# Kernel optimization log

Measured on AMD Instinct MI355X. Metric: run time of the kernel, lower is better.

Reference implementation:

```python
import jax, jax.numpy as jnp
import numpy as np

B, C, S, K, HEADS, P = 2, 64, 112, 7, 4, 3
DH = C // HEADS

def _na_idx(L, k):
    # NATTEN-style clamped windows: each query attends to k in-bounds neighbors
    i = np.arange(L)
    s = np.clip(i - k // 2, 0, L - k)
    nbr = s[:, None] + np.arange(k)[None, :]      # (L,k) absolute neighbor index
    rel = nbr - i[:, None] + (k - 1)              # (L,k) rel-pos-bias index in [0,2k-2]
    return jnp.asarray(nbr), jnp.asarray(rel)

def _ln(x, g, b, eps=1e-5):
    m = jnp.mean(x, -1, keepdims=True)
    v = jnp.mean(jnp.square(x - m), -1, keepdims=True)
    return (x - m) * jax.lax.rsqrt(v + eps) * g + b

def _conv(x, w, b):
    y = jax.lax.conv_general_dilated(x, w, (1, 1), [(P // 2, P // 2)] * 2,
                                     dimension_numbers=('NCHW', 'OIHW', 'NCHW'))
    return jnp.transpose(y + b[None, :, None, None], (0, 2, 3, 1))  # NHWC

def setup_inputs():
    key = jax.random.key(0)
    ks = jax.random.split(key, 24)
    r = lambda i, shape, s=0.02: jax.random.normal(ks[i], shape, jnp.float32) * s
    return {
        'xq': jax.random.normal(ks[0], (B, C, S, S), jnp.float32),
        'xkv': jax.random.normal(ks[1], (B, C, S, S), jnp.float32),
        'conv_w_s': r(2, (C, C, P, P)), 'conv_b_s': r(3, (C,), 0.01),
        'conv_w_l': r(4, (C, C, P, P)), 'conv_b_l': r(5, (C,), 0.01),
        'g_s': jnp.ones((C,), jnp.float32), 'b_s': jnp.zeros((C,), jnp.float32),
        'g_l': jnp.ones((C,), jnp.float32), 'b_l': jnp.zeros((C,), jnp.float32),
        'Wq': r(6, (C, C)), 'bq': r(7, (C,), 0.01),
        'Wk': r(8, (C, C)), 'bk': r(9, (C,), 0.01),
        'Wv': r(10, (C, C)), 'bv': r(11, (C,), 0.01),
        'Wo': r(12, (C, C)), 'bo': r(13, (C,), 0.01),
        'rpb': r(14, (HEADS, 2 * K - 1, 2 * K - 1)),
        'g_n': jnp.ones((C,), jnp.float32), 'b_n': jnp.zeros((C,), jnp.float32),
        'W1': r(15, (C, 2 * C)), 'b1': r(16, (2 * C,), 0.01),
        'W2': r(17, (2 * C, C)), 'b2': r(18, (C,), 0.01),
    }

def reference(xq, xkv, conv_w_s, conv_b_s, conv_w_l, conv_b_l, g_s, b_s, g_l, b_l,
              Wq, bq, Wk, bk, Wv, bv, Wo, bo, rpb, g_n, b_n, W1, b1, W2, b2):
    emb_q = _conv(xq, conv_w_s, conv_b_s)     # (B,H,W,C) overlap patch embed (q branch)
    emb_kv = _conv(xkv, conv_w_l, conv_b_l)   # (B,H,W,C)
    Hh, Ww = emb_q.shape[1], emb_q.shape[2]
    qn = _ln(emb_q, g_s, b_s)
    kvn = _ln(emb_kv, g_l, b_l)
    q = (qn @ Wq + bq).reshape(B, Hh, Ww, HEADS, DH)
    k = (kvn @ Wk + bk).reshape(B, Hh, Ww, HEADS, DH)
    v = (kvn @ Wv + bv).reshape(B, Hh, Ww, HEADS, DH)
    ni, ri = _na_idx(Hh, K)
    nj, rj = _na_idx(Ww, K)

    def gather(t):  # (B,H,W,h,d) -> (B,H,W,K*K,h,d) neighborhood windows
        t = t[:, ni]                                 # (B,H,K,W,h,d)
        t = t[:, :, :, nj]                           # (B,H,K,W,K,h,d)
        t = jnp.transpose(t, (0, 1, 3, 2, 4, 5, 6))  # (B,H,W,K,K,h,d)
        return t.reshape(B, Hh, Ww, K * K, HEADS, DH)

    kg, vg = gather(k), gather(v)
    logits = jnp.einsum('bijhd,bijnhd->bhijn', q, kg) * (DH ** -0.5)
    bias = rpb[:, ri]                                # (h,H,K,2K-1)
    bias = bias[:, :, :, rj]                         # (h,H,K,W,K)
    bias = jnp.transpose(bias, (0, 1, 3, 2, 4)).reshape(HEADS, Hh, Ww, K * K)
    attn = jax.nn.softmax(logits + bias[None], axis=-1)
    out = jnp.einsum('bhijn,bijnhd->bijhd', attn, vg).reshape(B, Hh, Ww, C)
    att = out @ Wo + bo + emb_kv                     # residual with kv embedding
    x = _ln(att, g_n, b_n)
    x = jax.nn.gelu(x @ W1 + b1, approximate=False) @ W2 + b2 + att
    return jnp.transpose(x, (0, 3, 1, 2))            # (B,C,H,W)
```

## Files before the change

### kernel.cpp

```cpp
#include <hip/hip_runtime.h>
#include <math.h>

#define SS 112
#define HW (SS*SS)
#define NPIX (2*HW)

typedef __bf16 v8bf __attribute__((ext_vector_type(8)));
typedef short  v8s  __attribute__((ext_vector_type(8)));
typedef float  v4f  __attribute__((ext_vector_type(4)));

__device__ __forceinline__ unsigned short f2bf(float f){
  unsigned u = __builtin_bit_cast(unsigned, f);
  u = (u + 0x7fffu + ((u >> 16) & 1u)) >> 16;
  return (unsigned short)u;
}
__device__ __forceinline__ unsigned cvt_pk_bf16(float lo, float hi){
  unsigned r;
  asm("v_cvt_pk_bf16_f32 %0, %1, %2" : "=v"(r) : "v"(lo), "v"(hi));
  return r;
}
__device__ __forceinline__ v8bf zero8(){
  v8s z = {0,0,0,0,0,0,0,0};
  return __builtin_bit_cast(v8bf, z);
}
__device__ __forceinline__ float gelu_fast(float x){
  float u = fmaf(0.044715f*x, x, 1.0f);
  float z = fminf(2.3021178f * x * u, 80.0f);
  float s = exp2f(z);
  return x * s * __builtin_amdgcn_rcpf(s + 1.0f);
}

__device__ __forceinline__ void pack_wconv(const float* __restrict__ w,
                                           unsigned short* __restrict__ WB, int idx){
  int lane = idx & 63, tslot = (idx >> 6) & 3, kk = idx >> 8;
  int tap = kk >> 1;
  int ic0 = ((kk & 1) << 5) + ((lane >> 4) << 3);
  int oc  = tslot*16 + (lane & 15);
  union { unsigned short u[8]; uint4 q; } pk;
  #pragma unroll
  for (int i = 0; i < 8; ++i) pk.u[i] = f2bf(w[(oc*64 + ic0 + i)*9 + tap]);
  ((uint4*)WB)[idx] = pk.q;
}
__device__ __forceinline__ void pack_wlin(const float* __restrict__ W,
                                          unsigned short* __restrict__ WB,
                                          int N, int idx){
  int lane = idx & 63;
  int tmp = idx >> 6;
  int tiles = N >> 4;
  int tslot = tmp % tiles;
  int kk = tmp / tiles;
  int k0 = kk*32 + ((lane >> 4) << 3);
  int oc = tslot*16 + (lane & 15);
  union { unsigned short u[8]; uint4 q; } pk;
  #pragma unroll
  for (int i = 0; i < 8; ++i) pk.u[i] = f2bf(W[(size_t)(k0 + i)*N + oc]);
  ((uint4*)WB)[idx] = pk.q;
}

__global__ __launch_bounds__(256) void k_prep(
    const float* __restrict__ xq, const float* __restrict__ xkv,
    const float* __restrict__ cws, const float* __restrict__ cwl,
    const float* __restrict__ Wq, const float* __restrict__ Wk,
    const float* __restrict__ Wv, const float* __restrict__ Wo,
    const float* __restrict__ W1, const float* __restrict__ W2,
    const float* __restrict__ rpb,
    unsigned short* __restrict__ WBs, unsigned short* __restrict__ WBl,
    unsigned short* __restrict__ WBq, unsigned short* __restrict__ WBk,
    unsigned short* __restrict__ WBv, unsigned short* __restrict__ WBo,
    unsigned short* __restrict__ WB1, unsigned short* __restrict__ WB2,
    float* __restrict__ rpb2g,
    unsigned short* __restrict__ xTq, unsigned short* __restrict__ xTkv)
{
  __shared__ float tile[64][68];
  const int blk = blockIdx.x, t = threadIdx.x;
  if (blk < 55){
    if      (blk < 18) pack_wconv(cws, WBs, blk*256 + t);
    else if (blk < 36) pack_wconv(cwl, WBl, (blk-18)*256 + t);
    else if (blk < 38) pack_wlin(Wq, WBq, 64,  (blk-36)*256 + t);
    else if (blk < 40) pack_wlin(Wk, WBk, 64,  (blk-38)*256 + t);
    else if (blk < 42) pack_wlin(Wv, WBv, 64,  (blk-40)*256 + t);
    else if (blk < 44) pack_wlin(Wo, WBo, 64,  (blk-42)*256 + t);
    else if (blk < 48) pack_wlin(W1, WB1, 128, (blk-44)*256 + t);
    else if (blk < 52) pack_wlin(W2, WB2, 64,  (blk-48)*256 + t);
    else {
      int idx = (blk-52)*256 + t;
      if (idx < 4*169) rpb2g[idx] = rpb[idx] * 1.4426950408889634f;
    }
    return;
  }
  const int blk2 = blk - 55;
  const int inst = blk2 >= (NPIX/64) ? 1 : 0;
  const float* x = inst ? xkv : xq;
  unsigned short* xT = inst ? xTkv : xTq;
  const int base = (blk2 - inst*(NPIX/64)) * 64;
  const int b = base / HW;
  const int r0 = base - b*HW;
  {
    const int c = t >> 2, xo = (t & 3) << 4;
    const float* src = x + ((size_t)(b*64 + c))*HW + r0 + xo;
    float4 v0 = ((const float4*)src)[0];
    float4 v1 = ((const float4*)src)[1];
    float4 v2 = ((const float4*)src)[2];
    float4 v3 = ((const float4*)src)[3];
    float* dst = &tile[c][xo];
    ((float4*)dst)[0] = v0; ((float4*)dst)[1] = v1;
    ((float4*)dst)[2] = v2; ((float4*)dst)[3] = v3;
  }
  __syncthreads();
  {
    const int px = t >> 2, co = (t & 3) << 4;
    union { unsigned short u[16]; uint4 q[2]; } pk;
    #pragma unroll
    for (int i = 0; i < 16; ++i) pk.u[i] = f2bf(tile[co + i][px]);
    uint4* dst = (uint4*)(xT + ((size_t)(base + px))*64 + co);
    dst[0] = pk.q[0]; dst[1] = pk.q[1];
  }
}

__global__ __launch_bounds__(256) void k_conv_all(
    const unsigned short* __restrict__ xTq, const unsigned short* __restrict__ xTkv,
    const unsigned short* __restrict__ WBs, const unsigned short* __restrict__ WBl,
    const float* __restrict__ cbs, const float* __restrict__ g_s, const float* __restrict__ b_s,
    const float* __restrict__ cbl, const float* __restrict__ g_l, const float* __restrict__ b_l,
    const unsigned short* __restrict__ WBq, const float* __restrict__ bq_,
    const unsigned short* __restrict__ WBk, const float* __restrict__ bk_,
    const unsigned short* __restrict__ WBv, const float* __restrict__ bv_,
    unsigned short* __restrict__ qb, unsigned short* __restrict__ kb,
    unsigned short* __restrict__ vT, float* __restrict__ emb)
{
  __shared__ unsigned short nlds[4][16*64];
  const int tid = threadIdx.x;
  const int wid = tid >> 6, l = tid & 63;
  const int g = l >> 4, c = l & 15;
  const int HALF = NPIX/64;
  const int inst = blockIdx.x >= HALF ? 1 : 0;
  const int P0 = ((blockIdx.x - inst*HALF)*4 + wid) * 16;

  const unsigned short* xT  = inst ? xTkv : xTq;
  const unsigned short* WBc = inst ? WBl : WBs;
  const float* cb    = inst ? cbl : cbs;
  const float* gamma = inst ? g_l : g_s;
  const float* beta  = inst ? b_l : b_s;

  const int p = P0 + c;
  const int b = p / HW, r = p - b*HW;
  const int py = r / SS, pxx = r - py*SS;
  const int pb64 = b*HW;

  float cbv[4], gv[4], bev[4];
  #pragma unroll
  for (int t = 0; t < 4; ++t){
    cbv[t] = cb[c + 16*t]; gv[t] = gamma[c + 16*t]; bev[t] = beta[c + 16*t];
  }

  v4f acc[4];
  #pragma unroll
  for (int t = 0; t < 4; ++t) acc[t] = (v4f){cbv[t], cbv[t], cbv[t], cbv[t]};

  const int icg = g << 3;
  #pragma unroll
  for (int kk = 0; kk < 18; ++kk){
    const int tap = kk >> 1;
    const int dy = tap/3 - 1, dx = tap - (tap/3)*3 - 1;
    const int icof = ((kk & 1) << 5) + icg;
    int yy = py + dy, xx = pxx + dx;
    bool ok = ((unsigned)yy < SS) && ((unsigned)xx < SS);
    v8bf a = zero8();
    if (ok) a = *(const v8bf*)(xT + ((size_t)(pb64 + yy*SS + xx))*64 + icof);
    #pragma unroll
    for (int t = 0; t < 4; ++t){
      v8bf bfr = *(const v8bf*)(WBc + ((size_t)((kk*4 + t)*64 + l))*8);
      acc[t] = __builtin_amdgcn_mfma_f32_16x16x32_bf16(a, bfr, acc[t], 0, 0, 0);
    }
  }

  if (inst){
    #pragma unroll
    for (int t = 0; t < 4; ++t)
      #pragma unroll
      for (int r2 = 0; r2 < 4; ++r2)
        emb[((size_t)(P0 + 4*g + r2))*64 + c + 16*t] = acc[t][r2];
  }

  {
    float mean[4], inv[4];
    #pragma unroll
    for (int r2 = 0; r2 < 4; ++r2){
      float s = acc[0][r2] + acc[1][r2] + acc[2][r2] + acc[3][r2];
      s += __shfl_xor(s, 1, 64); s += __shfl_xor(s, 2, 64);
      s += __shfl_xor(s, 4, 64); s += __shfl_xor(s, 8, 64);
      mean[r2] = s * (1.f/64.f);
      float d0 = acc[0][r2] - mean[r2], d1 = acc[1][r2] - mean[r2];
      float d2 = acc[2][r2] - mean[r2], d3 = acc[3][r2] - mean[r2];
      float vs = d0*d0 + d1*d1 + d2*d2 + d3*d3;
      vs += __shfl_xor(vs, 1, 64); vs += __shfl_xor(vs, 2, 64);
      vs += __shfl_xor(vs, 4, 64); vs += __shfl_xor(vs, 8, 64);
      inv[r2] = rsqrtf(vs * (1.f/64.f) + 1e-5f);
    }
    #pragma unroll
    for (int t = 0; t < 4; ++t){
      int c16 = 2*t + (c >> 3);
      #pragma unroll
      for (int r2 = 0; r2 < 4; r2 += 2){
        int row0 = 4*g + r2, row1 = row0 + 1;
        float n0 = (acc[t][r2]   - mean[r2])   * inv[r2]   * gv[t] + bev[t];
        float n1 = (acc[t][r2+1] - mean[r2+1]) * inv[r2+1] * gv[t] + bev[t];
        unsigned w = cvt_pk_bf16(n0, n1);
        nlds[wid][row0*64 + (((c16 ^ (row0 & 7)) << 3) | (c & 7))] = (unsigned short)(w & 0xffffu);
        nlds[wid][row1*64 + (((c16 ^ (row1 & 7)) << 3) | (c & 7))] = (unsigned short)(w >> 16);
      }
    }
  }

  #pragma unroll
  for (int which = 0; which < 2; ++which){
    if (which == 1 && !inst) break;
    const unsigned short* WB = which ? WBv : (inst ? WBk : WBq);
    const float* bias        = which ? bv_ : (inst ? bk_ : bq_);

    float pb[4];
    #pragma unroll
    for (int t = 0; t < 4; ++t) pb[t] = bias[c + 16*t];
    v4f pa[4];
    #pragma unroll
    for (int t = 0; t < 4; ++t) pa[t] = (v4f){pb[t], pb[t], pb[t], pb[t]};

    #pragma unroll
    for (int kk = 0; kk < 2; ++kk){
      v8bf av = *(const v8bf*)(nlds[wid] + c*64 + (((kk*4 + g) ^ (c & 7)) << 3));
      #pragma unroll
      for (int t = 0; t < 4; ++t){
        v8bf bfr = *(const v8bf*)(WB + ((size_t)((kk*4 + t)*64 + l))*8);
        pa[t] = __builtin_amdgcn_mfma_f32_16x16x32_bf16(av, bfr, pa[t], 0, 0, 0);
      }
    }
    if (which == 0){
      unsigned short* outp = inst ? kb : qb;
      #pragma unroll
      for (int t = 0; t < 4; ++t)
        #pragma unroll
        for (int r2 = 0; r2 < 4; r2 += 2){
          unsigned w = cvt_pk_bf16(pa[t][r2], pa[t][r2+1]);
          outp[((size_t)(P0 + 4*g + r2))*64 + c + 16*t]     = (unsigned short)(w & 0xffffu);
          outp[((size_t)(P0 + 4*g + r2+1))*64 + c + 16*t]   = (unsigned short)(w >> 16);
        }
    } else {
      #pragma unroll
      for (int t = 0; t < 4; ++t){
        uint2 w2;
        w2.x = cvt_pk_bf16(pa[t][0], pa[t][1]);
        w2.y = cvt_pk_bf16(pa[t][2], pa[t][3]);
        *(uint2*)(vT + (size_t)(c + 16*t)*NPIX + (P0 + 4*g)) = w2;
      }
    }
  }
}

__global__ __launch_bounds__(256) void k_natten_mfma(
    const unsigned short* __restrict__ q, const unsigned short* __restrict__ k,
    const unsigned short* __restrict__ vT, const float* __restrict__ rpb2g,
    unsigned short* __restrict__ out)
{
  const int l = threadIdx.x & 63;
  const int h = threadIdx.x >> 6;
  const int p0 = blockIdx.x * 16;
  const int b = p0 / HW, r0 = p0 - b*HW;
  const int i = r0 / SS, j0 = r0 - i*SS;
  const int c = l & 15, g = l >> 4;

  const int si = min(max(i - 3, 0), SS - 7);
  const int aj = (min(max(j0 - 3, 0), SS - 22)) & ~7;
  const int oi = si - i + 6;
  const int pbase = b*HW;

  const int j   = j0 + c;
  const int sjp = min(max(j - 3, 0), SS - 7);
  const int adj = 8*g + (aj - sjp);
  const float* bp = rpb2g + h*169 + oi*13 + (8*g + aj - j + 6);

  v8bf bq = zero8();
  if (g < 2) bq = *(const v8bf*)(q + (size_t)(p0 + c)*64 + h*16 + 8*g);

  float lt[14][4];
  const int arow = 8*(c >> 2) + (c & 3);
  #pragma unroll
  for (int tau = 0; tau < 14; ++tau){
    const int t = tau >> 1;
    int kpix = pbase + (si + t)*SS + aj + arow + 4*(tau & 1);
    kpix = min(kpix, NPIX - 1);
    v8bf ak = zero8();
    if (g < 2) ak = *(const v8bf*)(k + (size_t)kpix*64 + h*16 + 8*g);
    v4f a0 = {0.f,0.f,0.f,0.f};
    a0 = __builtin_amdgcn_mfma_f32_16x16x32_bf16(ak, bq, a0, 0, 0, 0);
    lt[tau][0]=a0[0]; lt[tau][1]=a0[1]; lt[tau][2]=a0[2]; lt[tau][3]=a0[3];
  }

  const float SC = 0.3606737602222409f;
  float mx4[4] = {-3e38f,-3e38f,-3e38f,-3e38f};
  #pragma unroll
  for (int tau = 0; tau < 14; ++tau){
    const int t = tau >> 1;
    #pragma unroll
    for (int r = 0; r < 4; ++r){
      const int cc = 4*(tau & 1) + r;
      float bias = bp[t*13 + cc];
      float lg = fmaf(lt[tau][r], SC, bias);
      lt[tau][r] = ((unsigned)(adj + cc) <= 6u) ? lg : -1e30f;
      mx4[r] = fmaxf(mx4[r], lt[tau][r]);
    }
  }
  float mx = fmaxf(fmaxf(mx4[0], mx4[1]), fmaxf(mx4[2], mx4[3]));
  mx = fmaxf(mx, __shfl_xor(mx, 16, 64));
  mx = fmaxf(mx, __shfl_xor(mx, 32, 64));
  float es4[4] = {0.f,0.f,0.f,0.f};
  #pragma unroll
  for (int tau = 0; tau < 14; ++tau)
    #pragma unroll
    for (int r = 0; r < 4; ++r){
      float p = exp2f(lt[tau][r] - mx);
      lt[tau][r] = p;
      es4[r] += p;
    }
  float es = (es4[0] + es4[1]) + (es4[2] + es4[3]);
  es += __shfl_xor(es, 16, 64);
  es += __shfl_xor(es, 32, 64);
  const float inv = 1.0f / es;

  const unsigned short* vrow = vT + (size_t)(h*16 + c)*NPIX;
  v4f oacc = {0.f,0.f,0.f,0.f};
  #pragma unroll
  for (int t = 0; t < 7; ++t){
    union { unsigned w[4]; v8bf bf; } pa;
    pa.w[0] = cvt_pk_bf16(lt[2*t][0]*inv,   lt[2*t][1]*inv);
    pa.w[1] = cvt_pk_bf16(lt[2*t][2]*inv,   lt[2*t][3]*inv);
    pa.w[2] = cvt_pk_bf16(lt[2*t+1][0]*inv, lt[2*t+1][1]*inv);
    pa.w[3] = cvt_pk_bf16(lt[2*t+1][2]*inv, lt[2*t+1][3]*inv);
    int vpixb = pbase + (si + t)*SS + aj + 8*g;
    vpixb = min(vpixb, NPIX - 8);
    v8bf bv = *(const v8bf*)(vrow + vpixb);
    oacc = __builtin_amdgcn_mfma_f32_16x16x32_bf16(pa.bf, bv, oacc, 0, 0, 0);
  }

  #pragma unroll
  for (int r = 0; r < 4; r += 2){
    unsigned w = cvt_pk_bf16(oacc[r], oacc[r+1]);
    out[(size_t)(p0 + 4*g + r)*64 + h*16 + c]     = (unsigned short)(w & 0xffffu);
    out[(size_t)(p0 + 4*g + r+1)*64 + h*16 + c]   = (unsigned short)(w >> 16);
  }
}

__global__ __launch_bounds__(256) void k_out_mfma(
    const unsigned short* __restrict__ ao, const float* __restrict__ emb,
    const unsigned short* __restrict__ WBo, const float* __restrict__ bo,
    const float* __restrict__ gn, const float* __restrict__ bn,
    const unsigned short* __restrict__ WB1, const float* __restrict__ b1,
    const unsigned short* __restrict__ WB2, const float* __restrict__ b2,
    float* __restrict__ outp)
{
  __shared__ unsigned short ylds[4][16*64];
  __shared__ unsigned short hlds[4][16*128];
  const int tid = threadIdx.x;
  const int wid = tid >> 6, l = tid & 63;
  const int g = l >> 4, c = l & 15;
  const int P0 = (blockIdx.x*4 + wid) * 16;
  const int b = P0 / HW;
  const int ijb = P0 - b*HW;

  v4f att[4];
  #pragma unroll
  for (int t = 0; t < 4; ++t){
    float bb = bo[c + 16*t];
    #pragma unroll
    for (int r = 0; r < 4; ++r)
      att[t][r] = bb + emb[((size_t)(P0 + 4*g + r))*64 + c + 16*t];
  }
  #pragma unroll
  for (int kk = 0; kk < 2; ++kk){
    v8bf a = *(const v8bf*)(ao + (size_t)(P0 + c)*64 + kk*32 + 8*g);
    #pragma unroll
    for (int t = 0; t < 4; ++t){
      v8bf bfr = *(const v8bf*)(WBo + ((size_t)((kk*4 + t)*64 + l))*8);
      att[t] = __builtin_amdgcn_mfma_f32_16x16x32_bf16(a, bfr, att[t], 0, 0, 0);
    }
  }

  {
    float gv[4], bev[4];
    #pragma unroll
    for (int t = 0; t < 4; ++t){ gv[t] = gn[c + 16*t]; bev[t] = bn[c + 16*t]; }
    float mean[4], inv[4];
    #pragma unroll
    for (int r = 0; r < 4; ++r){
      float s = att[0][r] + att[1][r] + att[2][r] + att[3][r];
      s += __shfl_xor(s, 1, 64); s += __shfl_xor(s, 2, 64);
      s += __shfl_xor(s, 4, 64); s += __shfl_xor(s, 8, 64);
      mean[r] = s * (1.f/64.f);
      float d0 = att[0][r] - mean[r], d1 = att[1][r] - mean[r];
      float d2 = att[2][r] - mean[r], d3 = att[3][r] - mean[r];
      float vs = d0*d0 + d1*d1 + d2*d2 + d3*d3;
      vs += __shfl_xor(vs, 1, 64); vs += __shfl_xor(vs, 2, 64);
      vs += __shfl_xor(vs, 4, 64); vs += __shfl_xor(vs, 8, 64);
      inv[r] = rsqrtf(vs * (1.f/64.f) + 1e-5f);
    }
    #pragma unroll
    for (int t = 0; t < 4; ++t){
      int c16 = 2*t + (c >> 3);
      #pragma unroll
      for (int r = 0; r < 4; r += 2){
        int row0 = 4*g + r, row1 = row0 + 1;
        float n0 = (att[t][r]   - mean[r])   * inv[r]   * gv[t] + bev[t];
        float n1 = (att[t][r+1] - mean[r+1]) * inv[r+1] * gv[t] + bev[t];
        unsigned w = cvt_pk_bf16(n0, n1);
        ylds[wid][row0*64 + (((c16 ^ (row0 & 7)) << 3) | (c & 7))] = (unsigned short)(w & 0xffffu);
        ylds[wid][row1*64 + (((c16 ^ (row1 & 7)) << 3) | (c & 7))] = (unsigned short)(w >> 16);
      }
    }
  }

  v4f hc[8];
  #pragma unroll
  for (int tt = 0; tt < 8; ++tt){
    float bb = b1[c + 16*tt];
    hc[tt] = (v4f){bb,bb,bb,bb};
  }
  #pragma unroll
  for (int kk = 0; kk < 2; ++kk){
    v8bf a = *(const v8bf*)(ylds[wid] + c*64 + (((kk*4 + g) ^ (c & 7)) << 3));
    #pragma unroll
    for (int tt = 0; tt < 8; ++tt){
      v8bf bfr = *(const v8bf*)(WB1 + ((size_t)((kk*8 + tt)*64 + l))*8);
      hc[tt] = __builtin_amdgcn_mfma_f32_16x16x32_bf16(a, bfr, hc[tt], 0, 0, 0);
    }
  }
  #pragma unroll
  for (int tt = 0; tt < 8; ++tt){
    int chunk = 2*tt + (c >> 3);
    #pragma unroll
    for (int r = 0; r < 4; r += 2){
      int row0 = 4*g + r, row1 = row0 + 1;
      int swz0 = (chunk & 8) | ((chunk & 7) ^ (row0 & 7));
      int swz1 = (chunk & 8) | ((chunk & 7) ^ (row1 & 7));
      unsigned w = cvt_pk_bf16(gelu_fast(hc[tt][r]), gelu_fast(hc[tt][r+1]));
      hlds[wid][row0*128 + swz0*8 + (c & 7)] = (unsigned short)(w & 0xffffu);
      hlds[wid][row1*128 + swz1*8 + (c & 7)] = (unsigned short)(w >> 16);
    }
  }

  v4f xc[4];
  #pragma unroll
  for (int t = 0; t < 4; ++t){
    float bb = b2[c + 16*t];
    #pragma unroll
    for (int r = 0; r < 4; ++r)
      xc[t][r] = bb + att[t][r];
  }
  #pragma unroll
  for (int kk = 0; kk < 4; ++kk){
    int chunk = 4*kk + g;
    int swz = (chunk & 8) | ((chunk & 7) ^ (c & 7));
    v8bf a = *(const v8bf*)(hlds[wid] + c*128 + swz*8);
    #pragma unroll
    for (int t = 0; t < 4; ++t){
      v8bf bfr = *(const v8bf*)(WB2 + ((size_t)((kk*4 + t)*64 + l))*8);
      xc[t] = __builtin_amdgcn_mfma_f32_16x16x32_bf16(a, bfr, xc[t], 0, 0, 0);
    }
  }
  #pragma unroll
  for (int t = 0; t < 4; ++t)
    #pragma unroll
    for (int r = 0; r < 4; ++r)
      outp[((size_t)(b*64 + c + 16*t))*HW + ijb + 4*g + r] = xc[t][r];
}

extern "C" void kernel_launch(void* const* d_in, const int* in_sizes, int n_in,
                              void* d_out, int out_size, void* d_ws, size_t ws_size,
                              hipStream_t stream) {
  const float* xq  = (const float*)d_in[0];
  const float* xkv = (const float*)d_in[1];
  const float* cws = (const float*)d_in[2];
  const float* cbs = (const float*)d_in[3];
  const float* cwl = (const float*)d_in[4];
  const float* cbl = (const float*)d_in[5];
  const float* g_s = (const float*)d_in[6];
  const float* b_s = (const float*)d_in[7];
  const float* g_l = (const float*)d_in[8];
  const float* b_l = (const float*)d_in[9];
  const float* Wq  = (const float*)d_in[10];
  const float* bq  = (const float*)d_in[11];
  const float* Wk  = (const float*)d_in[12];
  const float* bk  = (const float*)d_in[13];
  const float* Wv  = (const float*)d_in[14];
  const float* bv  = (const float*)d_in[15];
  const float* Wo  = (const float*)d_in[16];
  const float* bo  = (const float*)d_in[17];
  const float* rpb = (const float*)d_in[18];
  const float* g_n = (const float*)d_in[19];
  const float* b_n = (const float*)d_in[20];
  const float* W1  = (const float*)d_in[21];
  const float* b1  = (const float*)d_in[22];
  const float* W2  = (const float*)d_in[23];
  const float* b2  = (const float*)d_in[24];

  unsigned short* xTq  = (unsigned short*)d_ws;
  unsigned short* xTkv = xTq  + (size_t)NPIX*64;
  unsigned short* WBs  = xTkv + (size_t)NPIX*64;
  unsigned short* WBl  = WBs  + 36864;
  unsigned short* WBq  = WBl  + 36864;
  unsigned short* WBk  = WBq  + 4096;
  unsigned short* WBv  = WBk  + 4096;
  unsigned short* WBo  = WBv  + 4096;
  unsigned short* WB1  = WBo  + 4096;
  unsigned short* WB2  = WB1  + 8192;
  unsigned short* qb   = WB2  + 8192;
  unsigned short* kb   = qb   + (size_t)NPIX*64;
  unsigned short* vT   = kb   + (size_t)NPIX*64;
  unsigned short* aob  = vT   + (size_t)NPIX*64;
  float* emb   = (float*)(aob + (size_t)NPIX*64);
  float* rpb2a = emb + (size_t)NPIX*64;
  float* rpb2g = rpb2a + 64;

  hipLaunchKernelGGL(k_prep, dim3(55 + NPIX/32), dim3(256), 0, stream,
      xq, xkv, cws, cwl, Wq, Wk, Wv, Wo, W1, W2, rpb,
      WBs, WBl, WBq, WBk, WBv, WBo, WB1, WB2, rpb2g, xTq, xTkv);

  hipLaunchKernelGGL(k_conv_all, dim3(NPIX/32), dim3(256), 0, stream,
      xTq, xTkv, WBs, WBl,
      cbs, g_s, b_s, cbl, g_l, b_l,
      WBq, bq, WBk, bk, WBv, bv,
      qb, kb, vT, emb);

  hipLaunchKernelGGL(k_natten_mfma, dim3(NPIX/16), dim3(256), 0, stream,
      qb, kb, vT, rpb2g, aob);

  hipLaunchKernelGGL(k_out_mfma, dim3(NPIX/64), dim3(256), 0, stream,
      aob, emb, WBo, bo, g_n, b_n, WB1, b1, WB2, b2, (float*)d_out);
}
```

Measured before the change: 75.01 us.

## Fuse neighborhood attention with output projection and MLP into one kernel

```diff
diff --git a/kernel.cpp b/kernel.cpp
--- a/kernel.cpp
+++ b/kernel.cpp
@@ -29,6 +29,16 @@
   float s = exp2f(z);
   return x * s * __builtin_amdgcn_rcpf(s + 1.0f);
 }
+
+struct Params {
+  const float *xq, *xkv, *cws, *cwl, *Wq, *Wk, *Wv, *Wo, *W1, *W2, *rpb;
+  const float *cbs, *g_s, *b_s, *cbl, *g_l, *b_l;
+  const float *bq, *bk, *bv, *bo, *gn, *bn, *b1, *b2;
+  unsigned short *WBs, *WBl, *WBq, *WBk, *WBv, *WBo, *WB1, *WB2;
+  float *rpb2g;
+  unsigned short *xTq, *xTkv, *qb, *kb, *vT;
+  float *emb, *outp;
+};
 
 __device__ __forceinline__ void pack_wconv(const float* __restrict__ w,
                                            unsigned short* __restrict__ WB, int idx){
@@ -57,90 +67,70 @@
   ((uint4*)WB)[idx] = pk.q;
 }
 
-__global__ __launch_bounds__(256) void k_prep(
-    const float* __restrict__ xq, const float* __restrict__ xkv,
-    const float* __restrict__ cws, const float* __restrict__ cwl,
-    const float* __restrict__ Wq, const float* __restrict__ Wk,
-    const float* __restrict__ Wv, const float* __restrict__ Wo,
-    const float* __restrict__ W1, const float* __restrict__ W2,
-    const float* __restrict__ rpb,
-    unsigned short* __restrict__ WBs, unsigned short* __restrict__ WBl,
-    unsigned short* __restrict__ WBq, unsigned short* __restrict__ WBk,
-    unsigned short* __restrict__ WBv, unsigned short* __restrict__ WBo,
-    unsigned short* __restrict__ WB1, unsigned short* __restrict__ WB2,
-    float* __restrict__ rpb2g,
-    unsigned short* __restrict__ xTq, unsigned short* __restrict__ xTkv)
+__global__ __launch_bounds__(256) void k_prep_s(Params P)
 {
   __shared__ float tile[64][68];
-  const int blk = blockIdx.x, t = threadIdx.x;
-  if (blk < 55){
-    if      (blk < 18) pack_wconv(cws, WBs, blk*256 + t);
-    else if (blk < 36) pack_wconv(cwl, WBl, (blk-18)*256 + t);
-    else if (blk < 38) pack_wlin(Wq, WBq, 64,  (blk-36)*256 + t);
-    else if (blk < 40) pack_wlin(Wk, WBk, 64,  (blk-38)*256 + t);
-    else if (blk < 42) pack_wlin(Wv, WBv, 64,  (blk-40)*256 + t);
-    else if (blk < 44) pack_wlin(Wo, WBo, 64,  (blk-42)*256 + t);
-    else if (blk < 48) pack_wlin(W1, WB1, 128, (blk-44)*256 + t);
-    else if (blk < 52) pack_wlin(W2, WB2, 64,  (blk-48)*256 + t);
+  const int u = blockIdx.x, tid = threadIdx.x;
+  if (u >= 784){
+    const int pu = u - 784;
+    if      (pu < 18) pack_wconv(P.cws, P.WBs, pu*256 + tid);
+    else if (pu < 36) pack_wconv(P.cwl, P.WBl, (pu-18)*256 + tid);
+    else if (pu < 38) pack_wlin(P.Wq, P.WBq, 64,  (pu-36)*256 + tid);
+    else if (pu < 40) pack_wlin(P.Wk, P.WBk, 64,  (pu-38)*256 + tid);
+    else if (pu < 42) pack_wlin(P.Wv, P.WBv, 64,  (pu-40)*256 + tid);
+    else if (pu < 44) pack_wlin(P.Wo, P.WBo, 64,  (pu-42)*256 + tid);
+    else if (pu < 48) pack_wlin(P.W1, P.WB1, 128, (pu-44)*256 + tid);
+    else if (pu < 52) pack_wlin(P.W2, P.WB2, 64,  (pu-48)*256 + tid);
     else {
-      int idx = (blk-52)*256 + t;
-      if (idx < 4*169) rpb2g[idx] = rpb[idx] * 1.4426950408889634f;
+      int idx = (pu-52)*256 + tid;
+      if (idx < 4*169) P.rpb2g[idx] = P.rpb[idx] * 1.4426950408889634f;
     }
     return;
   }
-  const int blk2 = blk - 55;
-  const int inst = blk2 >= (NPIX/64) ? 1 : 0;
-  const float* x = inst ? xkv : xq;
-  unsigned short* xT = inst ? xTkv : xTq;
-  const int base = (blk2 - inst*(NPIX/64)) * 64;
+  const int inst = u >= 392 ? 1 : 0;
+  const float* x = inst ? P.xkv : P.xq;
+  unsigned short* xT = inst ? P.xTkv : P.xTq;
+  const int base = (u - inst*392) * 64;
   const int b = base / HW;
   const int r0 = base - b*HW;
   {
-    const int c = t >> 2, xo = (t & 3) << 4;
-    const float* src = x + ((size_t)(b*64 + c))*HW + r0 + xo;
+    const int cc = tid >> 2, xo = (tid & 3) << 4;
+    const float* src = x + ((size_t)(b*64 + cc))*HW + r0 + xo;
     float4 v0 = ((const float4*)src)[0];
     float4 v1 = ((const float4*)src)[1];
     float4 v2 = ((const float4*)src)[2];
     float4 v3 = ((const float4*)src)[3];
-    float* dst = &tile[c][xo];
+    float* dst = &tile[cc][xo];
     ((float4*)dst)[0] = v0; ((float4*)dst)[1] = v1;
     ((float4*)dst)[2] = v2; ((float4*)dst)[3] = v3;
   }
   __syncthreads();
   {
-    const int px = t >> 2, co = (t & 3) << 4;
-    union { unsigned short u[16]; uint4 q[2]; } pk;
-    #pragma unroll
-    for (int i = 0; i < 16; ++i) pk.u[i] = f2bf(tile[co + i][px]);
+    const int px = tid >> 2, co = (tid & 3) << 4;
+    union { unsigned short uu[16]; uint4 q[2]; } pk;
+    #pragma unroll
+    for (int i = 0; i < 16; ++i) pk.uu[i] = f2bf(tile[co + i][px]);
     uint4* dst = (uint4*)(xT + ((size_t)(base + px))*64 + co);
     dst[0] = pk.q[0]; dst[1] = pk.q[1];
   }
 }
 
-__global__ __launch_bounds__(256) void k_conv_all(
-    const unsigned short* __restrict__ xTq, const unsigned short* __restrict__ xTkv,
-    const unsigned short* __restrict__ WBs, const unsigned short* __restrict__ WBl,
-    const float* __restrict__ cbs, const float* __restrict__ g_s, const float* __restrict__ b_s,
-    const float* __restrict__ cbl, const float* __restrict__ g_l, const float* __restrict__ b_l,
-    const unsigned short* __restrict__ WBq, const float* __restrict__ bq_,
-    const unsigned short* __restrict__ WBk, const float* __restrict__ bk_,
-    const unsigned short* __restrict__ WBv, const float* __restrict__ bv_,
-    unsigned short* __restrict__ qb, unsigned short* __restrict__ kb,
-    unsigned short* __restrict__ vT, float* __restrict__ emb)
+__global__ __launch_bounds__(256) void k_conv_s(Params P)
 {
-  __shared__ unsigned short nlds[4][16*64];
+  __shared__ unsigned short nlds4[4][1024];
   const int tid = threadIdx.x;
   const int wid = tid >> 6, l = tid & 63;
   const int g = l >> 4, c = l & 15;
-  const int HALF = NPIX/64;
-  const int inst = blockIdx.x >= HALF ? 1 : 0;
-  const int P0 = ((blockIdx.x - inst*HALF)*4 + wid) * 16;
-
-  const unsigned short* xT  = inst ? xTkv : xTq;
-  const unsigned short* WBc = inst ? WBl : WBs;
-  const float* cb    = inst ? cbl : cbs;
-  const float* gamma = inst ? g_l : g_s;
-  const float* beta  = inst ? b_l : b_s;
+  unsigned short* nlds = nlds4[wid];
+  const int u = blockIdx.x;
+  const int inst = u >= 392 ? 1 : 0;
+  const int P0 = ((u - inst*392)*4 + wid) * 16;
+
+  const unsigned short* xT  = inst ? P.xTkv : P.xTq;
+  const unsigned short* WBc = inst ? P.WBl : P.WBs;
+  const float* cb    = inst ? P.cbl : P.cbs;
+  const float* gamma = inst ? P.g_l : P.g_s;
+  const float* beta  = inst ? P.b_l : P.b_s;
 
   const int p = P0 + c;
   const int b = p / HW, r = p - b*HW;
@@ -179,7 +169,7 @@
     for (int t = 0; t < 4; ++t)
       #pragma unroll
       for (int r2 = 0; r2 < 4; ++r2)
-        emb[((size_t)(P0 + 4*g + r2))*64 + c + 16*t] = acc[t][r2];
+        P.emb[((size_t)(P0 + 4*g + r2))*64 + c + 16*t] = acc[t][r2];
   }
 
   {
@@ -206,8 +196,8 @@
         float n0 = (acc[t][r2]   - mean[r2])   * inv[r2]   * gv[t] + bev[t];
         float n1 = (acc[t][r2+1] - mean[r2+1]) * inv[r2+1] * gv[t] + bev[t];
         unsigned w = cvt_pk_bf16(n0, n1);
-        nlds[wid][row0*64 + (((c16 ^ (row0 & 7)) << 3) | (c & 7))] = (unsigned short)(w & 0xffffu);
-        nlds[wid][row1*64 + (((c16 ^ (row1 & 7)) << 3) | (c & 7))] = (unsigned short)(w >> 16);
+        nlds[row0*64 + (((c16 ^ (row0 & 7)) << 3) | (c & 7))] = (unsigned short)(w & 0xffffu);
+        nlds[row1*64 + (((c16 ^ (row1 & 7)) << 3) | (c & 7))] = (unsigned short)(w >> 16);
       }
     }
   }
@@ -215,8 +205,8 @@
   #pragma unroll
   for (int which = 0; which < 2; ++which){
     if (which == 1 && !inst) break;
-    const unsigned short* WB = which ? WBv : (inst ? WBk : WBq);
-    const float* bias        = which ? bv_ : (inst ? bk_ : bq_);
+    const unsigned short* WB = which ? P.WBv : (inst ? P.WBk : P.WBq);
+    const float* bias        = which ? P.bv : (inst ? P.bk : P.bq);
 
     float pb[4];
     #pragma unroll
@@ -227,7 +217,7 @@
 
     #pragma unroll
     for (int kk = 0; kk < 2; ++kk){
-      v8bf av = *(const v8bf*)(nlds[wid] + c*64 + (((kk*4 + g) ^ (c & 7)) << 3));
+      v8bf av = *(const v8bf*)(nlds + c*64 + (((kk*4 + g) ^ (c & 7)) << 3));
       #pragma unroll
       for (int t = 0; t < 4; ++t){
         v8bf bfr = *(const v8bf*)(WB + ((size_t)((kk*4 + t)*64 + l))*8);
@@ -235,14 +225,14 @@
       }
     }
     if (which == 0){
-      unsigned short* outp = inst ? kb : qb;
+      unsigned short* outp = inst ? P.kb : P.qb;
       #pragma unroll
       for (int t = 0; t < 4; ++t)
         #pragma unroll
         for (int r2 = 0; r2 < 4; r2 += 2){
           unsigned w = cvt_pk_bf16(pa[t][r2], pa[t][r2+1]);
-          outp[((size_t)(P0 + 4*g + r2))*64 + c + 16*t]     = (unsigned short)(w & 0xffffu);
-          outp[((size_t)(P0 + 4*g + r2+1))*64 + c + 16*t]   = (unsigned short)(w >> 16);
+          outp[((size_t)(P0 + 4*g + r2))*64 + c + 16*t]   = (unsigned short)(w & 0xffffu);
+          outp[((size_t)(P0 + 4*g + r2+1))*64 + c + 16*t] = (unsigned short)(w >> 16);
         }
     } else {
       #pragma unroll
@@ -250,256 +240,253 @@
         uint2 w2;
         w2.x = cvt_pk_bf16(pa[t][0], pa[t][1]);
         w2.y = cvt_pk_bf16(pa[t][2], pa[t][3]);
-        *(uint2*)(vT + (size_t)(c + 16*t)*NPIX + (P0 + 4*g)) = w2;
-      }
-    }
-  }
-}
-
-__global__ __launch_bounds__(256) void k_natten_mfma(
-    const unsigned short* __restrict__ q, const unsigned short* __restrict__ k,
-    const unsigned short* __restrict__ vT, const float* __restrict__ rpb2g,
-    unsigned short* __restrict__ out)
+        *(uint2*)(P.vT + (size_t)(c + 16*t)*NPIX + (P0 + 4*g)) = w2;
+      }
+    }
+  }
+}
+
+__global__ __launch_bounds__(256) void k_nattenout(Params P)
 {
-  const int l = threadIdx.x & 63;
-  const int h = threadIdx.x >> 6;
-  const int p0 = blockIdx.x * 16;
-  const int b = p0 / HW, r0 = p0 - b*HW;
-  const int i = r0 / SS, j0 = r0 - i*SS;
-  const int c = l & 15, g = l >> 4;
-
-  const int si = min(max(i - 3, 0), SS - 7);
-  const int aj = (min(max(j0 - 3, 0), SS - 22)) & ~7;
-  const int oi = si - i + 6;
-  const int pbase = b*HW;
-
-  const int j   = j0 + c;
-  const int sjp = min(max(j - 3, 0), SS - 7);
-  const int adj = 8*g + (aj - sjp);
-  const float* bp = rpb2g + h*169 + oi*13 + (8*g + aj - j + 6);
-
-  v8bf bq = zero8();
-  if (g < 2) bq = *(const v8bf*)(q + (size_t)(p0 + c)*64 + h*16 + 8*g);
-
-  float lt[14][4];
-  const int arow = 8*(c >> 2) + (c & 3);
-  #pragma unroll
-  for (int tau = 0; tau < 14; ++tau){
-    const int t = tau >> 1;
-    int kpix = pbase + (si + t)*SS + aj + arow + 4*(tau & 1);
-    kpix = min(kpix, NPIX - 1);
-    v8bf ak = zero8();
-    if (g < 2) ak = *(const v8bf*)(k + (size_t)kpix*64 + h*16 + 8*g);
-    v4f a0 = {0.f,0.f,0.f,0.f};
-    a0 = __builtin_amdgcn_mfma_f32_16x16x32_bf16(ak, bq, a0, 0, 0, 0);
-    lt[tau][0]=a0[0]; lt[tau][1]=a0[1]; lt[tau][2]=a0[2]; lt[tau][3]=a0[3];
-  }
-
-  const float SC = 0.3606737602222409f;
-  float mx4[4] = {-3e38f,-3e38f,-3e38f,-3e38f};
-  #pragma unroll
-  for (int tau = 0; tau < 14; ++tau){
-    const int t = tau >> 1;
-    #pragma unroll
-    for (int r = 0; r < 4; ++r){
-      const int cc = 4*(tau & 1) + r;
-      float bias = bp[t*13 + cc];
-      float lg = fmaf(lt[tau][r], SC, bias);
-      lt[tau][r] = ((unsigned)(adj + cc) <= 6u) ? lg : -1e30f;
-      mx4[r] = fmaxf(mx4[r], lt[tau][r]);
-    }
-  }
-  float mx = fmaxf(fmaxf(mx4[0], mx4[1]), fmaxf(mx4[2], mx4[3]));
-  mx = fmaxf(mx, __shfl_xor(mx, 16, 64));
-  mx = fmaxf(mx, __shfl_xor(mx, 32, 64));
-  float es4[4] = {0.f,0.f,0.f,0.f};
-  #pragma unroll
-  for (int tau = 0; tau < 14; ++tau)
-    #pragma unroll
-    for (int r = 0; r < 4; ++r){
-      float p = exp2f(lt[tau][r] - mx);
-      lt[tau][r] = p;
-      es4[r] += p;
-    }
-  float es = (es4[0] + es4[1]) + (es4[2] + es4[3]);
-  es += __shfl_xor(es, 16, 64);
-  es += __shfl_xor(es, 32, 64);
-  const float inv = 1.0f / es;
-
-  const unsigned short* vrow = vT + (size_t)(h*16 + c)*NPIX;
-  v4f oacc = {0.f,0.f,0.f,0.f};
-  #pragma unroll
-  for (int t = 0; t < 7; ++t){
-    union { unsigned w[4]; v8bf bf; } pa;
-    pa.w[0] = cvt_pk_bf16(lt[2*t][0]*inv,   lt[2*t][1]*inv);
-    pa.w[1] = cvt_pk_bf16(lt[2*t][2]*inv,   lt[2*t][3]*inv);
-    pa.w[2] = cvt_pk_bf16(lt[2*t+1][0]*inv, lt[2*t+1][1]*inv);
-    pa.w[3] = cvt_pk_bf16(lt[2*t+1][2]*inv, lt[2*t+1][3]*inv);
-    int vpixb = pbase + (si + t)*SS + aj + 8*g;
-    vpixb = min(vpixb, NPIX - 8);
-    v8bf bv = *(const v8bf*)(vrow + vpixb);
-    oacc = __builtin_amdgcn_mfma_f32_16x16x32_bf16(pa.bf, bv, oacc, 0, 0, 0);
-  }
-
-  #pragma unroll
-  for (int r = 0; r < 4; r += 2){
-    unsigned w = cvt_pk_bf16(oacc[r], oacc[r+1]);
-    out[(size_t)(p0 + 4*g + r)*64 + h*16 + c]     = (unsigned short)(w & 0xffffu);
-    out[(size_t)(p0 + 4*g + r+1)*64 + h*16 + c]   = (unsigned short)(w >> 16);
-  }
-}
-
-__global__ __launch_bounds__(256) void k_out_mfma(
-    const unsigned short* __restrict__ ao, const float* __restrict__ emb,
-    const unsigned short* __restrict__ WBo, const float* __restrict__ bo,
-    const float* __restrict__ gn, const float* __restrict__ bn,
-    const unsigned short* __restrict__ WB1, const float* __restrict__ b1,
-    const unsigned short* __restrict__ WB2, const float* __restrict__ b2,
-    float* __restrict__ outp)
-{
-  __shared__ unsigned short ylds[4][16*64];
-  __shared__ unsigned short hlds[4][16*128];
+  __shared__ __align__(16) unsigned short alds[64*72];
+  __shared__ __align__(16) unsigned char smem[24576];
   const int tid = threadIdx.x;
   const int wid = tid >> 6, l = tid & 63;
   const int g = l >> 4, c = l & 15;
-  const int P0 = (blockIdx.x*4 + wid) * 16;
-  const int b = P0 / HW;
-  const int ijb = P0 - b*HW;
-
-  v4f att[4];
-  #pragma unroll
-  for (int t = 0; t < 4; ++t){
-    float bb = bo[c + 16*t];
-    #pragma unroll
-    for (int r = 0; r < 4; ++r)
-      att[t][r] = bb + emb[((size_t)(P0 + 4*g + r))*64 + c + 16*t];
-  }
-  #pragma unroll
-  for (int kk = 0; kk < 2; ++kk){
-    v8bf a = *(const v8bf*)(ao + (size_t)(P0 + c)*64 + kk*32 + 8*g);
+  const int blk = blockIdx.x;
+
+  for (int s = 0; s < 4; ++s){
+    const int u = blk*4 + s;
+    const int h = wid;
+    const int p0 = u * 16;
+    const int b = p0 / HW, r0 = p0 - b*HW;
+    const int i = r0 / SS, j0 = r0 - i*SS;
+
+    const int si = min(max(i - 3, 0), SS - 7);
+    const int aj = (min(max(j0 - 3, 0), SS - 22)) & ~7;
+    const int oi = si - i + 6;
+    const int pbase = b*HW;
+
+    const int j   = j0 + c;
+    const int sjp = min(max(j - 3, 0), SS - 7);
+    const int adj = 8*g + (aj - sjp);
+    const float* bp = P.rpb2g + h*169 + oi*13 + (8*g + aj - j + 6);
+
+    v8bf bq = zero8();
+    if (g < 2) bq = *(const v8bf*)(P.qb + (size_t)(p0 + c)*64 + h*16 + 8*g);
+
+    float lt[14][4];
+    const int arow = 8*(c >> 2) + (c & 3);
+    #pragma unroll
+    for (int tau = 0; tau < 14; ++tau){
+      const int t = tau >> 1;
+      int kpix = pbase + (si + t)*SS + aj + arow + 4*(tau & 1);
+      kpix = min(kpix, NPIX - 1);
+      v8bf ak = zero8();
+      if (g < 2) ak = *(const v8bf*)(P.kb + (size_t)kpix*64 + h*16 + 8*g);
+      v4f a0 = {0.f,0.f,0.f,0.f};
+      a0 = __builtin_amdgcn_mfma_f32_16x16x32_bf16(ak, bq, a0, 0, 0, 0);
+      lt[tau][0]=a0[0]; lt[tau][1]=a0[1]; lt[tau][2]=a0[2]; lt[tau][3]=a0[3];
+    }
+
+    const float SC = 0.3606737602222409f;
+    float mx4[4] = {-3e38f,-3e38f,-3e38f,-3e38f};
+    #pragma unroll
+    for (int tau = 0; tau < 14; ++tau){
+      const int t = tau >> 1;
+      #pragma unroll
+      for (int r = 0; r < 4; ++r){
+        const int cc = 4*(tau & 1) + r;
+        float bias = bp[t*13 + cc];
+        float lg = fmaf(lt[tau][r], SC, bias);
+        lt[tau][r] = ((unsigned)(adj + cc) <= 6u) ? lg : -1e30f;
+        mx4[r] = fmaxf(mx4[r], lt[tau][r]);
+      }
+    }
+    float mx = fmaxf(fmaxf(mx4[0], mx4[1]), fmaxf(mx4[2], mx4[3]));
+    mx = fmaxf(mx, __shfl_xor(mx, 16, 64));
+    mx = fmaxf(mx, __shfl_xor(mx, 32, 64));
+    float es4[4] = {0.f,0.f,0.f,0.f};
+    #pragma unroll
+    for (int tau = 0; tau < 14; ++tau)
+      #pragma unroll
+      for (int r = 0; r < 4; ++r){
+        float pexp = exp2f(lt[tau][r] - mx);
+        lt[tau][r] = pexp;
+        es4[r] += pexp;
+      }
+    float es = (es4[0] + es4[1]) + (es4[2] + es4[3]);
+    es += __shfl_xor(es, 16, 64);
+    es += __shfl_xor(es, 32, 64);
+    const float inv = 1.0f / es;
+
+    const unsigned short* vrow = P.vT + (size_t)(h*16 + c)*NPIX;
+    v4f oacc = {0.f,0.f,0.f,0.f};
+    #pragma unroll
+    for (int t = 0; t < 7; ++t){
+      union { unsigned w[4]; v8bf bf; } pa;
+      pa.w[0] = cvt_pk_bf16(lt[2*t][0]*inv,   lt[2*t][1]*inv);
+      pa.w[1] = cvt_pk_bf16(lt[2*t][2]*inv,   lt[2*t][3]*inv);
+      pa.w[2] = cvt_pk_bf16(lt[2*t+1][0]*inv, lt[2*t+1][1]*inv);
+      pa.w[3] = cvt_pk_bf16(lt[2*t+1][2]*inv, lt[2*t+1][3]*inv);
+      int vpixb = pbase + (si + t)*SS + aj + 8*g;
+      vpixb = min(vpixb, NPIX - 8);
+      v8bf bv = *(const v8bf*)(vrow + vpixb);
+      oacc = __builtin_amdgcn_mfma_f32_16x16x32_bf16(pa.bf, bv, oacc, 0, 0, 0);
+    }
+
+    #pragma unroll
+    for (int r = 0; r < 4; r += 2){
+      unsigned w = cvt_pk_bf16(oacc[r], oacc[r+1]);
+      alds[(s*16 + 4*g + r)*72   + h*16 + c] = (unsigned short)(w & 0xffffu);
+      alds[(s*16 + 4*g + r+1)*72 + h*16 + c] = (unsigned short)(w >> 16);
+    }
+  }
+  __syncthreads();
+
+  {
+    unsigned short* ylds = (unsigned short*)smem + wid*1024;
+    unsigned short* hlds = (unsigned short*)(smem + 8192) + wid*2048;
+    const int P0 = blk*64 + wid*16;
+    const int b = P0 / HW;
+    const int ijb = P0 - b*HW;
+
+    v4f att[4];
     #pragma unroll
     for (int t = 0; t < 4; ++t){
-      v8bf bfr = *(const v8bf*)(WBo + ((size_t)((kk*4 + t)*64 + l))*8);
-      att[t] = __builtin_amdgcn_mfma_f32_16x16x32_bf16(a, bfr, att[t], 0, 0, 0);
-    }
-  }
-
-  {
-    float gv[4], bev[4];
-    #pragma unroll
-    for (int t = 0; t < 4; ++t){ gv[t] = gn[c + 16*t]; bev[t] = bn[c + 16*t]; }
-    float mean[4], inv[4];
-    #pragma unroll
-    for (int r = 0; r < 4; ++r){
-      float s = att[0][r] + att[1][r] + att[2][r] + att[3][r];
-      s += __shfl_xor(s, 1, 64); s += __shfl_xor(s, 2, 64);
-      s += __shfl_xor(s, 4, 64); s += __shfl_xor(s, 8, 64);
-      mean[r] = s * (1.f/64.f);
-      float d0 = att[0][r] - mean[r], d1 = att[1][r] - mean[r];
-      float d2 = att[2][r] - mean[r], d3 = att[3][r] - mean[r];
-      float vs = d0*d0 + d1*d1 + d2*d2 + d3*d3;
-      vs += __shfl_xor(vs, 1, 64); vs += __shfl_xor(vs, 2, 64);
-      vs += __shfl_xor(vs, 4, 64); vs += __shfl_xor(vs, 8, 64);
-      inv[r] = rsqrtf(vs * (1.f/64.f) + 1e-5f);
-    }
-    #pragma unroll
-    for (int t = 0; t < 4; ++t){
-      int c16 = 2*t + (c >> 3);
+      float bb = P.bo[c + 16*t];
+      #pragma unroll
+      for (int r = 0; r < 4; ++r)
+        att[t][r] = bb + P.emb[((size_t)(P0 + 4*g + r))*64 + c + 16*t];
+    }
+    #pragma unroll
+    for (int kk = 0; kk < 2; ++kk){
+      v8bf a = *(const v8bf*)(alds + (wid*16 + c)*72 + kk*32 + 8*g);
+      #pragma unroll
+      for (int t = 0; t < 4; ++t){
+        v8bf bfr = *(const v8bf*)(P.WBo + ((size_t)((kk*4 + t)*64 + l))*8);
+        att[t] = __builtin_amdgcn_mfma_f32_16x16x32_bf16(a, bfr, att[t], 0, 0, 0);
+      }
+    }
+
+    {
+      float gv[4], bev[4];
+      #pragma unroll
+      for (int t = 0; t < 4; ++t){ gv[t] = P.gn[c + 16*t]; bev[t] = P.bn[c + 16*t]; }
+      float mean[4], inv[4];
+      #pragma unroll
+      for (int r = 0; r < 4; ++r){
+        float s = att[0][r] + att[1][r] + att[2][r] + att[3][r];
+        s += __shfl_xor(s, 1, 64); s += __shfl_xor(s, 2, 64);
+        s += __shfl_xor(s, 4, 64); s += __shfl_xor(s, 8, 64);
+        mean[r] = s * (1.f/64.f);
+        float d0 = att[0][r] - mean[r], d1 = att[1][r] - mean[r];
+        float d2 = att[2][r] - mean[r], d3 = att[3][r] - mean[r];
+        float vs = d0*d0 + d1*d1 + d2*d2 + d3*d3;
+        vs += __shfl_xor(vs, 1, 64); vs += __shfl_xor(vs, 2, 64);
+        vs += __shfl_xor(vs, 4, 64); vs += __shfl_xor(vs, 8, 64);
+        inv[r] = rsqrtf(vs * (1.f/64.f) + 1e-5f);
+      }
+      #pragma unroll
+      for (int t = 0; t < 4; ++t){
+        int c16 = 2*t + (c >> 3);
+        #pragma unroll
+        for (int r = 0; r < 4; r += 2){
+          int row0 = 4*g + r, row1 = row0 + 1;
+          float n0 = (att[t][r]   - mean[r])   * inv[r]   * gv[t] + bev[t];
+          float n1 = (att[t][r+1] - mean[r+1]) * inv[r+1] * gv[t] + bev[t];
+          unsigned w = cvt_pk_bf16(n0, n1);
+          ylds[row0*64 + (((c16 ^ (row0 & 7)) << 3) | (c & 7))] = (unsigned short)(w & 0xffffu);
+          ylds[row1*64 + (((c16 ^ (row1 & 7)) << 3) | (c & 7))] = (unsigned short)(w >> 16);
+        }
+      }
+    }
+
+    v4f hc[8];
+    #pragma unroll
+    for (int tt = 0; tt < 8; ++tt){
+      float bb = P.b1[c + 16*tt];
+      hc[tt] = (v4f){bb,bb,bb,bb};
+    }
+    #pragma unroll
+    for (int kk = 0; kk < 2; ++kk){
+      v8bf a = *(const v8bf*)(ylds + c*64 + (((kk*4 + g) ^ (c & 7)) << 3));
+      #pragma unroll
+      for (int tt = 0; tt < 8; ++tt){
+        v8bf bfr = *(const v8bf*)(P.WB1 + ((size_t)((kk*8 + tt)*64 + l))*8);
+        hc[tt] = __builtin_amdgcn_mfma_f32_16x16x32_bf16(a, bfr, hc[tt], 0, 0, 0);
+      }
+    }
+    #pragma unroll
+    for (int tt = 0; tt < 8; ++tt){
+      int chunk = 2*tt + (c >> 3);
       #pragma unroll
       for (int r = 0; r < 4; r += 2){
         int row0 = 4*g + r, row1 = row0 + 1;
-        float n0 = (att[t][r]   - mean[r])   * inv[r]   * gv[t] + bev[t];
-        float n1 = (att[t][r+1] - mean[r+1]) * inv[r+1] * gv[t] + bev[t];
-        unsigned w = cvt_pk_bf16(n0, n1);
-        ylds[wid][row0*64 + (((c16 ^ (row0 & 7)) << 3) | (c & 7))] = (unsigned short)(w & 0xffffu);
-        ylds[wid][row1*64 + (((c16 ^ (row1 & 7)) << 3) | (c & 7))] = (unsigned short)(w >> 16);
-      }
-    }
-  }
-
-  v4f hc[8];
-  #pragma unroll
-  for (int tt = 0; tt < 8; ++tt){
-    float bb = b1[c + 16*tt];
-    hc[tt] = (v4f){bb,bb,bb,bb};
-  }
-  #pragma unroll
-  for (int kk = 0; kk < 2; ++kk){
-    v8bf a = *(const v8bf*)(ylds[wid] + c*64 + (((kk*4 + g) ^ (c & 7)) << 3));
-    #pragma unroll
-    for (int tt = 0; tt < 8; ++tt){
-      v8bf bfr = *(const v8bf*)(WB1 + ((size_t)((kk*8 + tt)*64 + l))*8);
-      hc[tt] = __builtin_amdgcn_mfma_f32_16x16x32_bf16(a, bfr, hc[tt], 0, 0, 0);
-    }
-  }
-  #pragma unroll
-  for (int tt = 0; tt < 8; ++tt){
-    int chunk = 2*tt + (c >> 3);
-    #pragma unroll
-    for (int r = 0; r < 4; r += 2){
-      int row0 = 4*g + r, row1 = row0 + 1;
-      int swz0 = (chunk & 8) | ((chunk & 7) ^ (row0 & 7));
-      int swz1 = (chunk & 8) | ((chunk & 7) ^ (row1 & 7));
-      unsigned w = cvt_pk_bf16(gelu_fast(hc[tt][r]), gelu_fast(hc[tt][r+1]));
-      hlds[wid][row0*128 + swz0*8 + (c & 7)] = (unsigned short)(w & 0xffffu);
-      hlds[wid][row1*128 + swz1*8 + (c & 7)] = (unsigned short)(w >> 16);
-    }
-  }
-
-  v4f xc[4];
-  #pragma unroll
-  for (int t = 0; t < 4; ++t){
-    float bb = b2[c + 16*t];
-    #pragma unroll
-    for (int r = 0; r < 4; ++r)
-      xc[t][r] = bb + att[t][r];
-  }
-  #pragma unroll
-  for (int kk = 0; kk < 4; ++kk){
-    int chunk = 4*kk + g;
-    int swz = (chunk & 8) | ((chunk & 7) ^ (c & 7));
-    v8bf a = *(const v8bf*)(hlds[wid] + c*128 + swz*8);
+        int swz0 = (chunk & 8) | ((chunk & 7) ^ (row0 & 7));
+        int swz1 = (chunk & 8) | ((chunk & 7) ^ (row1 & 7));
+        unsigned w = cvt_pk_bf16(gelu_fast(hc[tt][r]), gelu_fast(hc[tt][r+1]));
+        hlds[row0*128 + swz0*8 + (c & 7)] = (unsigned short)(w & 0xffffu);
+        hlds[row1*128 + swz1*8 + (c & 7)] = (unsigned short)(w >> 16);
+      }
+    }
+
+    v4f xc[4];
     #pragma unroll
     for (int t = 0; t < 4; ++t){
-      v8bf bfr = *(const v8bf*)(WB2 + ((size_t)((kk*4 + t)*64 + l))*8);
-      xc[t] = __builtin_amdgcn_mfma_f32_16x16x32_bf16(a, bfr, xc[t], 0, 0, 0);
-    }
-  }
-  #pragma unroll
-  for (int t = 0; t < 4; ++t)
-    #pragma unroll
-    for (int r = 0; r < 4; ++r)
-      outp[((size_t)(b*64 + c + 16*t))*HW + ijb + 4*g + r] = xc[t][r];
+      float bb = P.b2[c + 16*t];
+      #pragma unroll
+      for (int r = 0; r < 4; ++r)
+        xc[t][r] = bb + att[t][r];
+    }
+    #pragma unroll
+    for (int kk = 0; kk < 4; ++kk){
+      int chunk = 4*kk + g;
+      int swz = (chunk & 8) | ((chunk & 7) ^ (c & 7));
+      v8bf a = *(const v8bf*)(hlds + c*128 + swz*8);
+      #pragma unroll
+      for (int t = 0; t < 4; ++t){
+        v8bf bfr = *(const v8bf*)(P.WB2 + ((size_t)((kk*4 + t)*64 + l))*8);
+        xc[t] = __builtin_amdgcn_mfma_f32_16x16x32_bf16(a, bfr, xc[t], 0, 0, 0);
+      }
+    }
+    #pragma unroll
+    for (int t = 0; t < 4; ++t)
+      #pragma unroll
+      for (int r = 0; r < 4; ++r)
+        P.outp[((size_t)(b*64 + c + 16*t))*HW + ijb + 4*g + r] = xc[t][r];
+  }
 }
 
 extern "C" void kernel_launch(void* const* d_in, const int* in_sizes, int n_in,
                               void* d_out, int out_size, void* d_ws, size_t ws_size,
                               hipStream_t stream) {
-  const float* xq  = (const float*)d_in[0];
-  const float* xkv = (const float*)d_in[1];
-  const float* cws = (const float*)d_in[2];
-  const float* cbs = (const float*)d_in[3];
-  const float* cwl = (const float*)d_in[4];
-  const float* cbl = (const float*)d_in[5];
-  const float* g_s = (const float*)d_in[6];
-  const float* b_s = (const float*)d_in[7];
-  const float* g_l = (const float*)d_in[8];
-  const float* b_l = (const float*)d_in[9];
-  const float* Wq  = (const float*)d_in[10];
-  const float* bq  = (const float*)d_in[11];
-  const float* Wk  = (const float*)d_in[12];
-  const float* bk  = (const float*)d_in[13];
-  const float* Wv  = (const float*)d_in[14];
-  const float* bv  = (const float*)d_in[15];
-  const float* Wo  = (const float*)d_in[16];
-  const float* bo  = (const float*)d_in[17];
-  const float* rpb = (const float*)d_in[18];
-  const float* g_n = (const float*)d_in[19];
-  const float* b_n = (const float*)d_in[20];
-  const float* W1  = (const float*)d_in[21];
-  const float* b1  = (const float*)d_in[22];
-  const float* W2  = (const float*)d_in[23];
-  const float* b2  = (const float*)d_in[24];
+  Params P;
+  P.xq  = (const float*)d_in[0];
+  P.xkv = (const float*)d_in[1];
+  P.cws = (const float*)d_in[2];
+  P.cbs = (const float*)d_in[3];
+  P.cwl = (const float*)d_in[4];
+  P.cbl = (const float*)d_in[5];
+  P.g_s = (const float*)d_in[6];
+  P.b_s = (const float*)d_in[7];
+  P.g_l = (const float*)d_in[8];
+  P.b_l = (const float*)d_in[9];
+  P.Wq  = (const float*)d_in[10];
+  P.bq  = (const float*)d_in[11];
+  P.Wk  = (const float*)d_in[12];
+  P.bk  = (const float*)d_in[13];
+  P.Wv  = (const float*)d_in[14];
+  P.bv  = (const float*)d_in[15];
+  P.Wo  = (const float*)d_in[16];
+  P.bo  = (const float*)d_in[17];
+  P.rpb = (const float*)d_in[18];
+  P.gn  = (const float*)d_in[19];
+  P.bn  = (const float*)d_in[20];
+  P.W1  = (const float*)d_in[21];
+  P.b1  = (const float*)d_in[22];
+  P.W2  = (const float*)d_in[23];
+  P.b2  = (const float*)d_in[24];
 
   unsigned short* xTq  = (unsigned short*)d_ws;
   unsigned short* xTkv = xTq  + (size_t)NPIX*64;
@@ -514,24 +501,17 @@
   unsigned short* qb   = WB2  + 8192;
   unsigned short* kb   = qb   + (size_t)NPIX*64;
   unsigned short* vT   = kb   + (size_t)NPIX*64;
-  unsigned short* aob  = vT   + (size_t)NPIX*64;
-  float* emb   = (float*)(aob + (size_t)NPIX*64);
+  float* emb   = (float*)(vT + (size_t)NPIX*64);
   float* rpb2a = emb + (size_t)NPIX*64;
   float* rpb2g = rpb2a + 64;
 
-  hipLaunchKernelGGL(k_prep, dim3(55 + NPIX/32), dim3(256), 0, stream,
-      xq, xkv, cws, cwl, Wq, Wk, Wv, Wo, W1, W2, rpb,
-      WBs, WBl, WBq, WBk, WBv, WBo, WB1, WB2, rpb2g, xTq, xTkv);
-
-  hipLaunchKernelGGL(k_conv_all, dim3(NPIX/32), dim3(256), 0, stream,
-      xTq, xTkv, WBs, WBl,
-      cbs, g_s, b_s, cbl, g_l, b_l,
-      WBq, bq, WBk, bk, WBv, bv,
-      qb, kb, vT, emb);
-
-  hipLaunchKernelGGL(k_natten_mfma, dim3(NPIX/16), dim3(256), 0, stream,
-      qb, kb, vT, rpb2g, aob);
-
-  hipLaunchKernelGGL(k_out_mfma, dim3(NPIX/64), dim3(256), 0, stream,
-      aob, emb, WBo, bo, g_n, b_n, WB1, b1, WB2, b2, (float*)d_out);
-}
+  P.WBs = WBs; P.WBl = WBl; P.WBq = WBq; P.WBk = WBk; P.WBv = WBv;
+  P.WBo = WBo; P.WB1 = WB1; P.WB2 = WB2;
+  P.rpb2g = rpb2g;
+  P.xTq = xTq; P.xTkv = xTkv; P.qb = qb; P.kb = kb; P.vT = vT;
+  P.emb = emb; P.outp = (float*)d_out;
+
+  hipLaunchKernelGGL(k_prep_s,    dim3(839), dim3(256), 0, stream, P);
+  hipLaunchKernelGGL(k_conv_s,    dim3(784), dim3(256), 0, stream, P);
+  hipLaunchKernelGGL(k_nattenout, dim3(392), dim3(256), 0, stream, P);
+}
```

Result: slower. 82.80 us (+10.4%).
